# Kernel tuning notes

Measured on AMD Instinct MI355X. Metric: run time of the kernel, lower is better.

Reference implementation:

```python
import jax, jax.numpy as jnp
import numpy as np

T, A, E, N, W, HID, FD = 4096, 1024, 512, 32768, 10, 150, 20
GI = 2 * A + E  # 2560
BINS = jnp.array([1, 2, 3, 4, 8, 16, 32, 64], dtype=jnp.int32)


def _mlp(x, W1, b1, W2, b2, W3, b3):
    # Score module: Linear->ReLU->Linear->ReLU->Linear->1 (dropout is a no-op in eval)
    h = jax.nn.relu(x @ W1 + b1)
    h = jax.nn.relu(h @ W2 + b2)
    return h @ W3 + b3


def setup_inputs() -> dict:
    key = jax.random.key(0)
    ks = jax.random.split(key, 20)
    s = 0.02
    inp = {
        "states": jax.random.normal(ks[0], (T, A), jnp.float32),
        "embeds": jax.random.normal(ks[1], (T, E), jnp.float32),
        "span_starts": jax.random.randint(ks[2], (N,), 0, T - W, jnp.int32),
        "span_widths": jax.random.randint(ks[3], (N,), 1, W + 1, jnp.int32),
        # attention Score params (input A)
        "Wa1": jax.random.normal(ks[4], (A, HID)) * s, "ba1": jnp.zeros((HID,)),
        "Wa2": jax.random.normal(ks[5], (HID, HID)) * s, "ba2": jnp.zeros((HID,)),
        "Wa3": jax.random.normal(ks[6], (HID, 1)) * s, "ba3": jnp.zeros((1,)),
        # width Feature embedding table: len(bins)+1 = 9 rows
        "width_emb": jax.random.normal(ks[7], (9, FD)) * s,
        # mention Score params (input GI + FD)
        "Ws1": jax.random.normal(ks[8], (GI + FD, HID)) * s, "bs1": jnp.zeros((HID,)),
        "Ws2": jax.random.normal(ks[9], (HID, HID)) * s, "bs2": jnp.zeros((HID,)),
        "Ws3": jax.random.normal(ks[10], (HID, 1)) * s, "bs3": jnp.zeros((1,)),
    }
    return inp


def reference(states, embeds, span_starts, span_widths,
              Wa1, ba1, Wa2, ba2, Wa3, ba3, width_emb,
              Ws1, bs1, Ws2, bs2, Ws3, bs3):
    # per-token attention logits  [T]
    attns = _mlp(states, Wa1, ba1, Wa2, ba2, Wa3, ba3).squeeze(-1)
    offs = jnp.arange(W)                                   # [W]
    pos = span_starts[:, None] + offs[None, :]             # [N, W]
    mask = offs[None, :] < span_widths[:, None]            # ragged span mask
    pos_c = jnp.clip(pos, 0, T - 1)
    logit = jnp.where(mask, attns[pos_c], -jnp.inf)        # [N, W]
    w = jax.nn.softmax(logit, axis=1)                      # per-span softmax
    attn_sum = jnp.einsum('nw,nwe->ne', w, embeds[pos_c])  # [N, E]
    ends = span_starts + span_widths - 1
    bin_idx = jnp.sum(span_widths[:, None] >= BINS[None, :], axis=1)
    size = width_emb[bin_idx]                              # [N, FD]
    g = jnp.concatenate([states[span_starts], states[ends], attn_sum, size], axis=1)
    scores = _mlp(g, Ws1, bs1, Ws2, bs2, Ws3, bs3).squeeze(-1)  # [N]
    return scores
```

## Files before the change

kernel.cpp:

```cpp
#include <hip/hip_runtime.h>
#include <math.h>

#define T_TOK 4096
#define A_DIM 1024
#define E_DIM 512
#define N_SPAN 32768
#define W_MAX 10
#define HID 150
#define FD 20

#define PR  160
#define KP2 160

#define WS_ATTNS 0
#define WS_PB    4096
#define WS_WPACK 1314816
#define PB_P0 0
#define PB_P1 655360
#define PB_P2 1310720
#define PB_P3 1966080
#define WP_ST  0
#define WP_V   491520
#define WP_A2  573440
#define WP_S2  599040
#define WP_WE1 624640
#define WP_TOTAL 626080

typedef short  bf16x8 __attribute__((ext_vector_type(8)));
typedef float  f32x4  __attribute__((ext_vector_type(4)));

__device__ __forceinline__ float4 ld4(const float* p) { return *(const float4*)p; }

__device__ __forceinline__ unsigned short f2bf(float f) {
    unsigned u = __float_as_uint(f);
    unsigned r = u + 0x7fffu + ((u >> 16) & 1u);
    return (unsigned short)(r >> 16);
}
__device__ __forceinline__ float bf2f(short s) {
    return __uint_as_float(((unsigned)(unsigned short)s) << 16);
}
__device__ __forceinline__ bf16x8 cvt_regs(const float4* a) {
    bf16x8 f;
    f[0] = (short)f2bf(a[0].x); f[1] = (short)f2bf(a[0].y);
    f[2] = (short)f2bf(a[0].z); f[3] = (short)f2bf(a[0].w);
    f[4] = (short)f2bf(a[1].x); f[5] = (short)f2bf(a[1].y);
    f[6] = (short)f2bf(a[1].z); f[7] = (short)f2bf(a[1].w);
    return f;
}

typedef const __attribute__((address_space(1))) unsigned int as1_u32;
typedef __attribute__((address_space(3))) unsigned int as3_u32;
__device__ __forceinline__ void dma16(const void* g, void* l) {
    __builtin_amdgcn_global_load_lds((as1_u32*)g, (as3_u32*)l, 16, 0, 0);
}
template<int N> __device__ __forceinline__ void waitv() {
    asm volatile("s_waitcnt vmcnt(%0)" :: "n"(N) : "memory");
}

__global__ __launch_bounds__(256) void prepack_kernel(
    const float* __restrict__ Wa1, const float* __restrict__ Ws1,
    const float* __restrict__ Wa2, const float* __restrict__ Ws2,
    const float* __restrict__ width_emb, unsigned short* __restrict__ wp)
{
    int idx = blockIdx.x * 256 + threadIdx.x;
    if (idx >= WP_TOTAL) return;
    float v = 0.f;
    if (idx < WP_V) {
        int gidx = idx / 163840, r = idx % 163840;
        int ngrp = r / 81920, r2 = r % 81920;
        int c = r2 / 2560, d = r2 % 2560;
        int n = d >> 5, qsw = (d >> 3) & 3, off = d & 7;
        int q = qsw ^ ((n >> 1) & 3);
        int k = c * 32 + q * 8 + off;
        int gn = ngrp * 80 + n;
        const float* W = (gidx == 0) ? Wa1 : Ws1 + (size_t)(gidx - 1) * 1024 * HID;
        if (gn < HID) v = W[(size_t)k * HID + gn];
    } else if (idx < WP_A2) {
        int r = idx - WP_V;
        int ngrp = r / 40960, r2 = r % 40960;
        int c = r2 / 2560, d = r2 % 2560;
        int n = d >> 5, qsw = (d >> 3) & 3, off = d & 7;
        int q = qsw ^ ((n >> 1) & 3);
        int k = c * 32 + q * 8 + off;
        int gn = ngrp * 80 + n;
        if (gn < HID) v = Ws1[(size_t)(2048 + k) * HID + gn];
    } else if (idx < WP_S2) {
        int e = idx - WP_A2;
        int n = e / KP2, k = e % KP2;
        if (n < HID && k < HID) v = Wa2[(size_t)k * HID + n];
    } else if (idx < WP_WE1) {
        int e = idx - WP_S2;
        int n = e / KP2, k = e % KP2;
        if (n < HID && k < HID) v = Ws2[(size_t)k * HID + n];
    } else {
        int e = idx - WP_WE1;
        int b = e / KP2, n = e % KP2;
        if (n < HID)
            for (int k = 0; k < FD; ++k)
                v = fmaf(width_emb[b * FD + k], Ws1[(size_t)(2560 + k) * HID + n], v);
    }
    wp[idx] = f2bf(v);
}

template<int NC>
__device__ __forceinline__ void gemm_dma(
    const float* __restrict__ aPtr, const unsigned short* __restrict__ srcB,
    unsigned short (*__restrict__ bufB)[2560],
    int lane, int l15, int quad, f32x4 (&acc)[5])
{
    const int swz = (quad ^ ((l15 >> 1) & 3)) * 8;
    float4 aR[3][2];
#define DMAB(c) { _Pragma("unroll")                                          \
        for (int i = 0; i < 5; ++i)                                          \
            dma16(srcB + (size_t)(c) * 2560 + i * 512 + lane * 8,            \
                  &bufB[(c) % 3][i * 512]); }
#define LDA(c) { aR[(c) % 3][0] = ld4(aPtr + (c) * 32);                      \
                 aR[(c) % 3][1] = ld4(aPtr + (c) * 32 + 4); }
    DMAB(0); LDA(0);
    DMAB(1); LDA(1);
#pragma unroll
    for (int c = 0; c < NC; ++c) {
        if (c + 2 < NC) { DMAB(c + 2); LDA(c + 2); }
        if (c + 2 < NC)      waitv<14>();
        else if (c + 1 < NC) waitv<7>();
        else                 waitv<0>();
        bf16x8 af = cvt_regs(aR[c % 3]);
        const unsigned short* bb = &bufB[c % 3][0];
#pragma unroll
        for (int t = 0; t < 5; ++t) {
            bf16x8 bf = *(const bf16x8*)(bb + t * 512 + l15 * 32 + swz);
            acc[t] = __builtin_amdgcn_mfma_f32_16x16x32_bf16(af, bf, acc[t], 0, 0, 0);
        }
    }
#undef DMAB
#undef LDA
}

__global__ __launch_bounds__(64) void token_kernel(
    const float* __restrict__ states, const float* __restrict__ embeds,
    const unsigned short* __restrict__ wp, unsigned short* __restrict__ Pb)
{
    __shared__ __align__(16) unsigned short bufB[3][2560];

    const int lane = threadIdx.x, l15 = lane & 15, quad = lane >> 4;
    const int task = blockIdx.x;

    f32x4 acc[5];
#pragma unroll
    for (int t = 0; t < 5; ++t)
#pragma unroll
        for (int i = 0; i < 4; ++i) acc[t][i] = 0.f;

    int m0, gidx, ngrp;
    if (task < 1536) {
        m0 = (task / 6) * 16;
        const int sub = task % 6;
        gidx = sub >> 1;
        ngrp = sub & 1;
        const float* aPtr = states + (size_t)(m0 + l15) * A_DIM + quad * 8;
        const unsigned short* srcB = wp + WP_ST + gidx * 163840 + ngrp * 81920;
        gemm_dma<32>(aPtr, srcB, bufB, lane, l15, quad, acc);
    } else {
        const int e = task - 1536;
        m0 = (e >> 1) * 16;
        ngrp = e & 1;
        gidx = 3;
        const float* aPtr = embeds + (size_t)(m0 + l15) * E_DIM + quad * 8;
        const unsigned short* srcB = wp + WP_V + ngrp * 40960;
        gemm_dma<16>(aPtr, srcB, bufB, lane, l15, quad, acc);
    }

    unsigned short* Pg = Pb + (size_t)gidx * 655360;
#pragma unroll
    for (int t = 0; t < 5; ++t) {
        const int col = ngrp * 80 + t * 16 + l15;
#pragma unroll
        for (int i = 0; i < 4; ++i)
            Pg[(size_t)(m0 + quad * 4 + i) * PR + col] =
                (col < HID) ? f2bf(acc[t][i]) : (unsigned short)0;
    }
}

__global__ __launch_bounds__(64) void attn_tail_kernel(
    const unsigned short* __restrict__ P0, const float* __restrict__ ba1,
    const unsigned short* __restrict__ wp, const float* __restrict__ ba2,
    const float* __restrict__ Wa3, const float* __restrict__ ba3,
    float* __restrict__ attns)
{
    const int t0 = blockIdx.x * 16;
    const int lane = threadIdx.x, l15 = lane & 15, quad = lane >> 4;

    f32x4 acc[10];
#pragma unroll
    for (int nt = 0; nt < 10; ++nt)
#pragma unroll
        for (int i = 0; i < 4; ++i) acc[nt][i] = 0.f;

    const unsigned short* prow = P0 + (size_t)(t0 + l15) * PR;
    const unsigned short* bb = wp + WP_A2 + l15 * KP2 + quad * 8;

#pragma unroll
    for (int c = 0; c < 5; ++c) {
        const int k0 = c * 32;
        const int kk = k0 + quad * 8;
        bf16x8 raw = *(const bf16x8*)(prow + kk);
        bf16x8 af;
#pragma unroll
        for (int j = 0; j < 8; ++j) {
            const float b = (kk + j < HID) ? ba1[kk + j] : 0.f;
            af[j] = (short)f2bf(fmaxf(bf2f(raw[j]) + b, 0.f));
        }
#pragma unroll
        for (int nt = 0; nt < 10; ++nt) {
            bf16x8 bf = *(const bf16x8*)(bb + nt * 16 * KP2 + k0);
            acc[nt] = __builtin_amdgcn_mfma_f32_16x16x32_bf16(af, bf, acc[nt], 0, 0, 0);
        }
    }

    float sc[4] = {0.f, 0.f, 0.f, 0.f};
#pragma unroll
    for (int nt = 0; nt < 10; ++nt) {
        const int col = nt * 16 + l15;
        const float w3 = (col < HID) ? Wa3[col] : 0.f;
        const float b2 = (col < HID) ? ba2[col] : 0.f;
#pragma unroll
        for (int i = 0; i < 4; ++i)
            sc[i] = fmaf(fmaxf(acc[nt][i] + b2, 0.f), w3, sc[i]);
    }
#pragma unroll
    for (int off = 8; off >= 1; off >>= 1)
#pragma unroll
        for (int i = 0; i < 4; ++i) sc[i] += __shfl_down(sc[i], off, 16);
    if (l15 == 0) {
        const float b3 = ba3[0];
#pragma unroll
        for (int i = 0; i < 4; ++i) attns[t0 + quad * 4 + i] = sc[i] + b3;
    }
}

__global__ __launch_bounds__(256) void span_kernel(
    const unsigned short* __restrict__ Pb, const float* __restrict__ attns,
    const unsigned short* __restrict__ wp,
    const int* __restrict__ span_starts, const int* __restrict__ span_widths,
    const float* __restrict__ bs1, const float* __restrict__ bs2,
    const float* __restrict__ Ws3, const float* __restrict__ bs3,
    float* __restrict__ out)
{
    __shared__ unsigned short sHb[32][168];
    __shared__ float s_wgt[32][W_MAX];
    __shared__ int s_st[32], s_wd[32], s_bin[32];
    __shared__ float sPart[4][32];
    __shared__ float sb1[KP2];

    const int tid = threadIdx.x;
    const int n0s = blockIdx.x * 32;

    if (tid < KP2) sb1[tid] = (tid < HID) ? bs1[tid] : 0.f;
    if (tid < 32) {
        int st = span_starts[n0s + tid], wd = span_widths[n0s + tid];
        s_st[tid] = st; s_wd[tid] = wd;
        s_bin[tid] = (wd >= 1) + (wd >= 2) + (wd >= 3) + (wd >= 4) +
                     (wd >= 8) + (wd >= 16) + (wd >= 32) + (wd >= 64);
        float lg[W_MAX];
        float m = -1e30f;
#pragma unroll
        for (int w = 0; w < W_MAX; ++w)
            if (w < wd) { float a = attns[st + w]; lg[w] = a; m = fmaxf(m, a); }
        float sum = 0.f;
#pragma unroll
        for (int w = 0; w < W_MAX; ++w) {
            float e = (w < wd) ? __expf(lg[w] - m) : 0.f;
            lg[w] = e; sum += e;
        }
        float inv = 1.f / sum;
#pragma unroll
        for (int w = 0; w < W_MAX; ++w) s_wgt[tid][w] = lg[w] * inv;
    }
    __syncthreads();

    {
        const unsigned short* P1b = Pb + PB_P1;
        const unsigned short* P2b = Pb + PB_P2;
        const unsigned short* P3b = Pb + PB_P3;
        const unsigned short* WEb = wp + WP_WE1;
        const int s = tid >> 3, jl = tid & 7;
        const int st = s_st[s], wd = s_wd[s];
        const size_t rs = (size_t)st * PR;
        const size_t re = (size_t)(st + wd - 1) * PR;
        const size_t rb = (size_t)s_bin[s] * PR;
        for (int c = jl; c < 20; c += 8) {
            const int j = c * 8;
            bf16x8 u1 = *(const bf16x8*)(P1b + rs + j);
            bf16x8 u2 = *(const bf16x8*)(P2b + re + j);
            bf16x8 uw = *(const bf16x8*)(WEb + rb + j);
            float acc[8];
#pragma unroll
            for (int i = 0; i < 8; ++i)
                acc[i] = bf2f(u1[i]) + bf2f(u2[i]) + bf2f(uw[i]) + sb1[j + i];
#pragma unroll
            for (int w = 0; w < W_MAX; ++w) {
                if (w < wd) {
                    float wt = s_wgt[s][w];
                    bf16x8 uv = *(const bf16x8*)(P3b + rs + (size_t)w * PR + j);
#pragma unroll
                    for (int i = 0; i < 8; ++i)
                        acc[i] = fmaf(wt, bf2f(uv[i]), acc[i]);
                }
            }
            bf16x8 pk;
#pragma unroll
            for (int i = 0; i < 8; ++i) pk[i] = (short)f2bf(fmaxf(acc[i], 0.f));
            *(bf16x8*)&sHb[s][j] = pk;
        }
    }
    __syncthreads();

    const int wv = tid >> 6, lane = tid & 63, l15 = lane & 15, quad = lane >> 4;
    const int nb = (wv < 2) ? wv * 3 : 6 + (wv - 2) * 2;
    const int cnt = (wv < 2) ? 3 : 2;

    f32x4 a2[2][3];
#pragma unroll
    for (int mt = 0; mt < 2; ++mt)
#pragma unroll
        for (int t = 0; t < 3; ++t)
#pragma unroll
            for (int i = 0; i < 4; ++i) a2[mt][t][i] = 0.f;

#pragma unroll
    for (int c = 0; c < 5; ++c) {
        int k0 = c * 32;
        bf16x8 af0 = *(const bf16x8*)&sHb[l15][k0 + quad * 8];
        bf16x8 af1 = *(const bf16x8*)&sHb[16 + l15][k0 + quad * 8];
#pragma unroll
        for (int t = 0; t < 3; ++t) {
            if (t < cnt) {
                bf16x8 b = *(const bf16x8*)(wp + WP_S2 +
                            (size_t)((nb + t) * 16 + l15) * KP2 + k0 + quad * 8);
                a2[0][t] = __builtin_amdgcn_mfma_f32_16x16x32_bf16(af0, b, a2[0][t], 0, 0, 0);
                a2[1][t] = __builtin_amdgcn_mfma_f32_16x16x32_bf16(af1, b, a2[1][t], 0, 0, 0);
            }
        }
    }

    float sc[2][4];
#pragma unroll
    for (int mt = 0; mt < 2; ++mt)
#pragma unroll
        for (int i = 0; i < 4; ++i) sc[mt][i] = 0.f;
#pragma unroll
    for (int t = 0; t < 3; ++t) {
        if (t < cnt) {
            int col = (nb + t) * 16 + l15;
            float w3 = (col < HID) ? Ws3[col] : 0.f;
            float b2 = (col < HID) ? bs2[col] : 0.f;
#pragma unroll
            for (int mt = 0; mt < 2; ++mt)
#pragma unroll
                for (int i = 0; i < 4; ++i)
                    sc[mt][i] = fmaf(fmaxf(a2[mt][t][i] + b2, 0.f), w3, sc[mt][i]);
        }
    }
#pragma unroll
    for (int off = 8; off >= 1; off >>= 1)
#pragma unroll
        for (int mt = 0; mt < 2; ++mt)
#pragma unroll
            for (int i = 0; i < 4; ++i)
                sc[mt][i] += __shfl_down(sc[mt][i], off, 16);
    if (l15 == 0) {
#pragma unroll
        for (int mt = 0; mt < 2; ++mt)
#pragma unroll
            for (int i = 0; i < 4; ++i)
                sPart[wv][mt * 16 + quad * 4 + i] = sc[mt][i];
    }
    __syncthreads();
    if (tid < 32)
        out[n0s + tid] = sPart[0][tid] + sPart[1][tid] + sPart[2][tid] +
                         sPart[3][tid] + bs3[0];
}

extern "C" void kernel_launch(void* const* d_in, const int* in_sizes, int n_in,
                              void* d_out, int out_size, void* d_ws, size_t ws_size,
                              hipStream_t stream)
{
    const float* states      = (const float*)d_in[0];
    const float* embeds      = (const float*)d_in[1];
    const int*   span_starts = (const int*)d_in[2];
    const int*   span_widths = (const int*)d_in[3];
    const float* Wa1 = (const float*)d_in[4];
    const float* ba1 = (const float*)d_in[5];
    const float* Wa2 = (const float*)d_in[6];
    const float* ba2 = (const float*)d_in[7];
    const float* Wa3 = (const float*)d_in[8];
    const float* ba3 = (const float*)d_in[9];
    const float* width_emb = (const float*)d_in[10];
    const float* Ws1 = (const float*)d_in[11];
    const float* bs1 = (const float*)d_in[12];
    const float* Ws2 = (const float*)d_in[13];
    const float* bs2 = (const float*)d_in[14];
    const float* Ws3 = (const float*)d_in[15];
    const float* bs3 = (const float*)d_in[16];
    float* out = (float*)d_out;

    float* ws    = (float*)d_ws;
    float* attns = ws + WS_ATTNS;
    unsigned short* Pb    = (unsigned short*)(ws + WS_PB);
    unsigned short* wpack = (unsigned short*)(ws + WS_WPACK);

    hipLaunchKernelGGL(prepack_kernel, dim3((WP_TOTAL + 255) / 256), dim3(256), 0, stream,
                       Wa1, Ws1, Wa2, Ws2, width_emb, wpack);
    hipLaunchKernelGGL(token_kernel, dim3(2048), dim3(64), 0, stream,
                       states, embeds, wpack, Pb);
    hipLaunchKernelGGL(attn_tail_kernel, dim3(T_TOK / 16), dim3(64), 0, stream,
                       Pb + PB_P0, ba1, wpack, ba2, Wa3, ba3, attns);
    hipLaunchKernelGGL(span_kernel, dim3(N_SPAN / 32), dim3(256), 0, stream,
                       Pb, attns, wpack, span_starts, span_widths,
                       bs1, bs2, Ws3, bs3, out);
}
```

Measured before the change: 151.2 us.

## Process two 16-row M tiles per block in token GEMM to reuse B tiles

Each block of the token projection kernel now computes 32 rows instead of 16, holding two sets of accumulators and issuing two MFMAs per B fragment read from LDS. This halves the number of blocks and halves the total weight DMA traffic into LDS per output row. In exchange it doubles the accumulator and A-register footprint per thread, needs adjusted wait counts, and cuts the grid to 1024 single-wave blocks, which may lower occupancy and latency hiding.

Result: no change. 151.2 us (+0.0%).

```diff
diff --git a/kernel.cpp b/kernel.cpp
--- a/kernel.cpp
+++ b/kernel.cpp
@@ -104,32 +104,38 @@
 
 template<int NC>
 __device__ __forceinline__ void gemm_dma(
-    const float* __restrict__ aPtr, const unsigned short* __restrict__ srcB,
+    const float* __restrict__ aPtr,
+    const unsigned short* __restrict__ srcB,
     unsigned short (*__restrict__ bufB)[2560],
-    int lane, int l15, int quad, f32x4 (&acc)[5])
-{
+    int lane, int l15, int quad, f32x4 (&acc)[2][5])
+{
+    constexpr int K = NC * 32;
     const int swz = (quad ^ ((l15 >> 1) & 3)) * 8;
-    float4 aR[3][2];
+    float4 aR[3][4];
 #define DMAB(c) { _Pragma("unroll")                                          \
         for (int i = 0; i < 5; ++i)                                          \
             dma16(srcB + (size_t)(c) * 2560 + i * 512 + lane * 8,            \
                   &bufB[(c) % 3][i * 512]); }
 #define LDA(c) { aR[(c) % 3][0] = ld4(aPtr + (c) * 32);                      \
-                 aR[(c) % 3][1] = ld4(aPtr + (c) * 32 + 4); }
+                 aR[(c) % 3][1] = ld4(aPtr + (c) * 32 + 4);                  \
+                 aR[(c) % 3][2] = ld4(aPtr + 16 * K + (c) * 32);             \
+                 aR[(c) % 3][3] = ld4(aPtr + 16 * K + (c) * 32 + 4); }
     DMAB(0); LDA(0);
     DMAB(1); LDA(1);
 #pragma unroll
     for (int c = 0; c < NC; ++c) {
         if (c + 2 < NC) { DMAB(c + 2); LDA(c + 2); }
-        if (c + 2 < NC)      waitv<14>();
-        else if (c + 1 < NC) waitv<7>();
+        if (c + 2 < NC)      waitv<18>();
+        else if (c + 1 < NC) waitv<9>();
         else                 waitv<0>();
-        bf16x8 af = cvt_regs(aR[c % 3]);
+        bf16x8 af0 = cvt_regs(&aR[c % 3][0]);
+        bf16x8 af1 = cvt_regs(&aR[c % 3][2]);
         const unsigned short* bb = &bufB[c % 3][0];
 #pragma unroll
         for (int t = 0; t < 5; ++t) {
             bf16x8 bf = *(const bf16x8*)(bb + t * 512 + l15 * 32 + swz);
-            acc[t] = __builtin_amdgcn_mfma_f32_16x16x32_bf16(af, bf, acc[t], 0, 0, 0);
+            acc[0][t] = __builtin_amdgcn_mfma_f32_16x16x32_bf16(af0, bf, acc[0][t], 0, 0, 0);
+            acc[1][t] = __builtin_amdgcn_mfma_f32_16x16x32_bf16(af1, bf, acc[1][t], 0, 0, 0);
         }
     }
 #undef DMAB
@@ -145,15 +151,17 @@
     const int lane = threadIdx.x, l15 = lane & 15, quad = lane >> 4;
     const int task = blockIdx.x;
 
-    f32x4 acc[5];
-#pragma unroll
-    for (int t = 0; t < 5; ++t)
-#pragma unroll
-        for (int i = 0; i < 4; ++i) acc[t][i] = 0.f;
+    f32x4 acc[2][5];
+#pragma unroll
+    for (int mt = 0; mt < 2; ++mt)
+#pragma unroll
+        for (int t = 0; t < 5; ++t)
+#pragma unroll
+            for (int i = 0; i < 4; ++i) acc[mt][t][i] = 0.f;
 
     int m0, gidx, ngrp;
-    if (task < 1536) {
-        m0 = (task / 6) * 16;
+    if (task < 768) {
+        m0 = (task / 6) * 32;
         const int sub = task % 6;
         gidx = sub >> 1;
         ngrp = sub & 1;
@@ -161,8 +169,8 @@
         const unsigned short* srcB = wp + WP_ST + gidx * 163840 + ngrp * 81920;
         gemm_dma<32>(aPtr, srcB, bufB, lane, l15, quad, acc);
     } else {
-        const int e = task - 1536;
-        m0 = (e >> 1) * 16;
+        const int e = task - 768;
+        m0 = (e >> 1) * 32;
         ngrp = e & 1;
         gidx = 3;
         const float* aPtr = embeds + (size_t)(m0 + l15) * E_DIM + quad * 8;
@@ -172,12 +180,16 @@
 
     unsigned short* Pg = Pb + (size_t)gidx * 655360;
 #pragma unroll
-    for (int t = 0; t < 5; ++t) {
-        const int col = ngrp * 80 + t * 16 + l15;
-#pragma unroll
-        for (int i = 0; i < 4; ++i)
-            Pg[(size_t)(m0 + quad * 4 + i) * PR + col] =
-                (col < HID) ? f2bf(acc[t][i]) : (unsigned short)0;
+    for (int mt = 0; mt < 2; ++mt) {
+        const int rowb = m0 + mt * 16 + quad * 4;
+#pragma unroll
+        for (int t = 0; t < 5; ++t) {
+            const int col = ngrp * 80 + t * 16 + l15;
+#pragma unroll
+            for (int i = 0; i < 4; ++i)
+                Pg[(size_t)(rowb + i) * PR + col] =
+                    (col < HID) ? f2bf(acc[mt][t][i]) : (unsigned short)0;
+        }
     }
 }
 
@@ -411,7 +423,7 @@
 
     hipLaunchKernelGGL(prepack_kernel, dim3((WP_TOTAL + 255) / 256), dim3(256), 0, stream,
                        Wa1, Ws1, Wa2, Ws2, width_emb, wpack);
-    hipLaunchKernelGGL(token_kernel, dim3(2048), dim3(64), 0, stream,
+    hipLaunchKernelGGL(token_kernel, dim3(1024), dim3(64), 0, stream,
                        states, embeds, wpack, Pb);
     hipLaunchKernelGGL(attn_tail_kernel, dim3(T_TOK / 16), dim3(64), 0, stream,
                        Pb + PB_P0, ba1, wpack, ba2, Wa3, ba3, attns);
```
